# Kernel tuning notes

Hardware: AMD Instinct MI355X
Metric: run time of the kernel (lower is better)

Reference implementation:

```python
import math
import jax, jax.numpy as jnp
import numpy as np

FACTOR = 5  # must match init_kwargs factor


def setup_inputs() -> dict:
    key = jax.random.key(0)
    B, L, H, D = 4, 2048, 16, 64
    k1, k2, k3, k4 = jax.random.split(key, 4)
    q = jax.random.normal(k1, (B, L, H, D), jnp.float32)
    k = jax.random.normal(k2, (B, L, H, D), jnp.float32)
    v = jax.random.normal(k3, (B, L, H, D), jnp.float32)
    sample_k = min(FACTOR * int(np.ceil(np.log(L))), L)  # = 40
    sample_idx = jax.random.randint(k4, (L, sample_k), 0, L)
    return {"q": q, "k": k, "v": v, "sample_idx": sample_idx, "attn_mask": 0}


def reference(q, k, v, sample_idx, attn_mask):
    B, L_q, H, D = q.shape
    L_k = k.shape[1]
    qh = jnp.swapaxes(q, 1, 2)  # [B,H,L_q,D]
    kh = jnp.swapaxes(k, 1, 2)  # [B,H,L_k,D]
    vh = jnp.swapaxes(v, 1, 2)  # [B,H,L_k,D]

    u_top = min(FACTOR * int(np.ceil(np.log(L_q))), L_q)

    # --- _prob_qk: sampled QK scores and sparsity measure M ---
    # k_s[b,h,q,s,d] = kh[b,h,sample_idx[q,s],d]  (per-query random key sample)
    k_s = kh[:, :, sample_idx, :]                       # [B,H,L_q,S,D]
    qk_sample = jnp.einsum('bhqd,bhqsd->bhqs', qh, k_s)  # [B,H,L_q,S]
    M = qk_sample.max(axis=-1) - qk_sample.sum(axis=-1) / L_k  # [B,H,L_q]
    _, M_top = jax.lax.top_k(M, u_top)                   # [B,H,u]

    # gather the top-u queries
    q_red = jnp.take_along_axis(qh, M_top[..., None], axis=2)  # [B,H,u,D]

    # dense scores of selected queries against all keys
    scores = jnp.einsum('bhud,bhkd->bhuk', q_red, kh) / math.sqrt(D)
    attn = jax.nn.softmax(scores, axis=-1)                     # [B,H,u,L_k]
    ctx = jnp.einsum('bhuk,bhkd->bhud', attn, vh)              # [B,H,u,D]

    # scatter context back into v at the selected query rows (RHS uses original v,
    # matching torch fancy-index assignment semantics)
    b_idx = jnp.arange(B)[:, None, None]
    h_idx = jnp.arange(H)[None, :, None]
    out = vh.at[b_idx, h_idx, M_top].set(ctx)
    return jnp.swapaxes(out, 1, 2)  # [B,L,H,D]
```

## Files before the change

### kernel.cpp

```cpp
#include <hip/hip_runtime.h>
#include <hip/hip_bf16.h>
#include <float.h>
#include <math.h>

constexpr int B = 4;
constexpr int L = 2048;
constexpr int H = 16;
constexpr int D = 64;
constexpr int U = 40;
constexpr int UHB = 20;
constexpr int KROWS = 128;
constexpr int NRCH = 16;
constexpr int LPB = 16;
constexpr int CPB2 = 2048;

typedef float floatx4 __attribute__((ext_vector_type(4)));

template<int SKC>
__global__ __launch_bounds__(256) void compute_M_kernel2(const float* __restrict__ q,
                                                         const float* __restrict__ k,
                                                         const int* __restrict__ sidx,
                                                         float* __restrict__ M) {
    int blk = blockIdx.x;
    int xcd = blk & 7;
    int rest = blk >> 3;
    int bh_hi = rest & 7;
    int chunk = rest >> 3;
    int bh = bh_hi * 8 + xcd;
    int b = bh >> 4, h = bh & 15;

    int t = threadIdx.x;
    int lg = t >> 4;
    int dg = t & 15;

    __shared__ int s_idx[LPB * SKC];
    for (int i = t; i < LPB * SKC; i += 256)
        s_idx[i] = sidx[(size_t)(chunk * LPB) * SKC + i];
    __syncthreads();

    int l = chunk * LPB + lg;
    floatx4 qv = __builtin_nontemporal_load(
        reinterpret_cast<const floatx4*>(q + ((size_t)(b * L + l) * H + h) * D + dg * 4));

    float mx = -FLT_MAX;
    float sm = 0.f;
    #pragma unroll 4
    for (int s = 0; s < SKC; ++s) {
        int kidx = s_idx[lg * SKC + s];
        floatx4 kv = *reinterpret_cast<const floatx4*>(
            k + ((size_t)(b * L + kidx) * H + h) * D + dg * 4);
        float p = qv.x * kv.x + qv.y * kv.y + qv.z * kv.z + qv.w * kv.w;
        #pragma unroll
        for (int off = 8; off >= 1; off >>= 1) p += __shfl_xor(p, off, 16);
        mx = fmaxf(mx, p);
        sm += p;
    }
    if (dg == 0) {
        M[(size_t)bh * L + l] = mx - sm * (1.0f / (float)L);
    }
}

__global__ __launch_bounds__(256) void compute_M_kernel(const float* __restrict__ q,
                                                        const float* __restrict__ k,
                                                        const int* __restrict__ sidx,
                                                        float* __restrict__ M, int SK) {
    int bl = blockIdx.x;
    int b = bl / L;
    int l = bl % L;
    int t = threadIdx.x;
    int h = t >> 4;
    int dg = t & 15;

    const float* qrow = q + ((size_t)(b * L + l)) * H * D + h * D + dg * 4;
    float4 qv = *reinterpret_cast<const float4*>(qrow);

    float mx = -FLT_MAX;
    float sm = 0.f;
    for (int s = 0; s < SK; ++s) {
        int kidx = sidx[l * SK + s];
        const float* krow = k + ((size_t)(b * L + kidx)) * H * D + h * D + dg * 4;
        float4 kv = *reinterpret_cast<const float4*>(krow);
        float p = qv.x * kv.x + qv.y * kv.y + qv.z * kv.z + qv.w * kv.w;
        #pragma unroll
        for (int off = 8; off >= 1; off >>= 1) p += __shfl_xor(p, off, 16);
        mx = fmaxf(mx, p);
        sm += p;
    }
    if (dg == 0) {
        M[((size_t)(b * H + h)) * L + l] = mx - sm * (1.0f / (float)L);
    }
}

__global__ __launch_bounds__(256) void topk_copy_kernel(const float* __restrict__ M,
                                                        int* __restrict__ Mtop,
                                                        const float* __restrict__ v,
                                                        float* __restrict__ out, int n4) {
    int blk = blockIdx.x;
    int t = threadIdx.x;

    if (blk >= B * H) {
        int i = (blk - B * H) * 256 + t;
        int stride = CPB2 * 256;
        const floatx4* src = reinterpret_cast<const floatx4*>(v);
        floatx4* dst = reinterpret_cast<floatx4*>(out);
        for (; i < n4; i += stride) {
            floatx4 x = __builtin_nontemporal_load(src + i);
            __builtin_nontemporal_store(x, dst + i);
        }
        return;
    }
    if (t >= 64) return;

    int bh = blk;
    int lane = t;
    const float* m = M + (size_t)bh * L;

    float v_[32];
    #pragma unroll
    for (int j = 0; j < 32; ++j) v_[j] = m[j * 64 + lane];

    for (int u = 0; u < U; ++u) {
        float bv = -FLT_MAX;
        int bi = 0x7fffffff;
        #pragma unroll
        for (int j = 0; j < 32; ++j) {
            int idx = j * 64 + lane;
            bool take = (v_[j] > bv) || (v_[j] == bv && idx < bi);
            bv = take ? v_[j] : bv;
            bi = take ? idx : bi;
        }
        #pragma unroll
        for (int off = 1; off < 64; off <<= 1) {
            float ov = __shfl_xor(bv, off);
            int   oi = __shfl_xor(bi, off);
            bool take = (ov > bv) || (ov == bv && oi < bi);
            bv = take ? ov : bv;
            bi = take ? oi : bi;
        }
        if (lane == 0) Mtop[bh * U + u] = bi;
        #pragma unroll
        for (int j = 0; j < 32; ++j) {
            if (bi == j * 64 + lane) v_[j] = -FLT_MAX;
        }
    }
}

__global__ __launch_bounds__(256) void flash2_kernel(
        const float* __restrict__ q, const float* __restrict__ k,
        const float* __restrict__ v, const int* __restrict__ Mtop,
        float* __restrict__ pl, float* __restrict__ pacc) {
    int blk = blockIdx.x;
    int xcd = blk & 7;
    int bh = ((blk >> 3) & 7) * 8 + xcd;
    int rest = blk >> 6;
    int rch = rest >> 1;
    int uhalf = rest & 1;
    int b = bh >> 4, h = bh & 15;
    int t = threadIdx.x;

    __shared__ __align__(16) float qs[UHB][D];
    __shared__ __align__(16) float pe[UHB][KROWS];
    __shared__ float redl[4][10];

    for (int i = t; i < UHB * D; i += 256) {
        int u = i >> 6, dd = i & 63;
        int qi = Mtop[bh * U + uhalf * UHB + u];
        qs[u][dd] = q[((size_t)(b * L + qi) * H + h) * D + dd];
    }
    __syncthreads();

    int tq = t >> 7;
    int rl = t & 127;
    int w = t >> 6;

    int r = rch * KROWS + rl;
    const float4* krow = reinterpret_cast<const float4*>(k + ((size_t)(b * L + r) * H + h) * D);

    float s[10];
    #pragma unroll
    for (int uu = 0; uu < 10; ++uu) s[uu] = 0.f;
    #pragma unroll 4
    for (int j = 0; j < 16; ++j) {
        float4 kj = krow[j];
        #pragma unroll
        for (int uu = 0; uu < 10; ++uu) {
            float4 qj = reinterpret_cast<const float4*>(qs[tq * 10 + uu])[j];
            s[uu] = fmaf(kj.x, qj.x, fmaf(kj.y, qj.y, fmaf(kj.z, qj.z, fmaf(kj.w, qj.w, s[uu]))));
        }
    }

    #pragma unroll
    for (int uu = 0; uu < 10; ++uu) {
        float e = __expf(s[uu] * 0.125f);
        pe[tq * 10 + uu][rl] = e;
        float ls = e;
        #pragma unroll
        for (int off = 1; off < 64; off <<= 1) ls += __shfl_xor(ls, off);
        if ((t & 63) == 0) redl[w][uu] = ls;
    }
    __syncthreads();

    int d = t & 63;
    int ug = t >> 6;
    const float* vb = v + ((size_t)(b * L + rch * KROWS) * H + h) * D + d;
    float acc[5];
    #pragma unroll
    for (int uu = 0; uu < 5; ++uu) acc[uu] = 0.f;
    #pragma unroll 2
    for (int row = 0; row < KROWS; row += 4) {
        float v0 = vb[(size_t)(row    ) * (H * D)];
        float v1 = vb[(size_t)(row + 1) * (H * D)];
        float v2 = vb[(size_t)(row + 2) * (H * D)];
        float v3 = vb[(size_t)(row + 3) * (H * D)];
        #pragma unroll
        for (int uu = 0; uu < 5; ++uu) {
            float4 p4 = *reinterpret_cast<const float4*>(&pe[ug * 5 + uu][row]);
            acc[uu] = fmaf(p4.x, v0, fmaf(p4.y, v1, fmaf(p4.z, v2, fmaf(p4.w, v3, acc[uu]))));
        }
    }
    size_t pb0 = (size_t)bh * U + uhalf * UHB;
    #pragma unroll
    for (int uu = 0; uu < 5; ++uu) {
        pacc[((pb0 + ug * 5 + uu) * NRCH + rch) * 64 + d] = acc[uu];
    }
    if (t < UHB) {
        int tqo = t / 10, uu = t % 10;
        float plv = redl[tqo * 2][uu] + redl[tqo * 2 + 1][uu];
        pl[(pb0 + t) * NRCH + rch] = plv;
    }
}

__global__ __launch_bounds__(256) void flash_merge_kernel(
        const float* __restrict__ pl, const float* __restrict__ pacc,
        const int* __restrict__ Mtop, float* __restrict__ out) {
    int idx = blockIdx.x * 256 + threadIdx.x;
    int dd = idx & 63;
    int bhu = idx >> 6;
    int bh = bhu / U;
    int b = bh / H, h = bh % H;

    float Lsum = 0.f;
    #pragma unroll
    for (int c = 0; c < NRCH; ++c) Lsum += pl[bhu * NRCH + c];

    float acc = 0.f;
    #pragma unroll
    for (int c = 0; c < NRCH; ++c)
        acc += pacc[((size_t)bhu * NRCH + c) * 64 + dd];

    int qi = Mtop[bhu];
    out[((size_t)(b * L + qi) * H + h) * D + dd] = acc / Lsum;
}

__global__ __launch_bounds__(256) void attn_kernel_fallback(
        const float* __restrict__ q, const float* __restrict__ k,
        const float* __restrict__ v, const int* __restrict__ Mtop,
        float* __restrict__ out) {
    int blk = blockIdx.x;
    int bh = blk / U;
    int u = blk % U;
    int b = bh / H;
    int h = bh % H;
    int qi = Mtop[bh * U + u];

    __shared__ float sc[L];
    __shared__ float qsf[D];
    __shared__ float red[4];
    __shared__ float ctx_s[4][D];

    int t = threadIdx.x;
    if (t < D) qsf[t] = q[((size_t)(b * L + qi)) * H * D + h * D + t];
    __syncthreads();

    float lm = -FLT_MAX;
    for (int i = t; i < L; i += 256) {
        const float* krow = k + ((size_t)(b * L + i)) * H * D + h * D;
        float acc = 0.f;
        #pragma unroll
        for (int dd = 0; dd < D; ++dd) acc += qsf[dd] * krow[dd];
        acc *= 0.125f;
        sc[i] = acc;
        lm = fmaxf(lm, acc);
    }
    #pragma unroll
    for (int off = 32; off >= 1; off >>= 1) lm = fmaxf(lm, __shfl_xor(lm, off));
    if ((t & 63) == 0) red[t >> 6] = lm;
    __syncthreads();
    float gm = fmaxf(fmaxf(red[0], red[1]), fmaxf(red[2], red[3]));

    float ls = 0.f;
    for (int i = t; i < L; i += 256) {
        float e = expf(sc[i] - gm);
        sc[i] = e;
        ls += e;
    }
    #pragma unroll
    for (int off = 32; off >= 1; off >>= 1) ls += __shfl_xor(ls, off);
    __syncthreads();
    if ((t & 63) == 0) red[t >> 6] = ls;
    __syncthreads();
    float inv = 1.0f / (red[0] + red[1] + red[2] + red[3]);

    int d = t & 63;
    int g = t >> 6;
    float acc = 0.f;
    for (int i = g; i < L; i += 4) {
        acc += sc[i] * v[((size_t)(b * L + i)) * H * D + h * D + d];
    }
    ctx_s[g][d] = acc;
    __syncthreads();
    if (g == 0) {
        float c = (ctx_s[0][d] + ctx_s[1][d] + ctx_s[2][d] + ctx_s[3][d]) * inv;
        out[((size_t)(b * L + qi)) * H * D + h * D + d] = c;
    }
}

extern "C" void kernel_launch(void* const* d_in, const int* in_sizes, int n_in,
                              void* d_out, int out_size, void* d_ws, size_t ws_size,
                              hipStream_t stream) {
    const float* q = (const float*)d_in[0];
    const float* k = (const float*)d_in[1];
    const float* v = (const float*)d_in[2];
    const int* sidx = (const int*)d_in[3];
    float* out = (float*)d_out;

    int SK = in_sizes[3] / L;

    size_t offM = 0;
    size_t offMtop = offM + (size_t)B * H * L * sizeof(float);
    size_t offPl = (offMtop + (size_t)B * H * U * sizeof(int) + 255) & ~(size_t)255;
    size_t offPacc = (offPl + (size_t)B * H * U * NRCH * sizeof(float) + 255) & ~(size_t)255;
    size_t needFlash = offPacc + (size_t)B * H * U * NRCH * 64 * sizeof(float);

    float* M = (float*)((char*)d_ws + offM);
    int* Mtop = (int*)((char*)d_ws + offMtop);
    float* pl = (float*)((char*)d_ws + offPl);
    float* pacc = (float*)((char*)d_ws + offPacc);

    int n4 = (B * L * H * D) / 4;

    if (SK == 40) {
        compute_M_kernel2<40><<<B * H * (L / LPB), 256, 0, stream>>>(q, k, sidx, M);
    } else {
        compute_M_kernel<<<B * L, 256, 0, stream>>>(q, k, sidx, M, SK);
    }

    topk_copy_kernel<<<B * H + CPB2, 256, 0, stream>>>(M, Mtop, v, out, n4);

    if (ws_size >= needFlash) {
        flash2_kernel<<<B * H * NRCH * 2, 256, 0, stream>>>(q, k, v, Mtop, pl, pacc);
        flash_merge_kernel<<<B * H * U * 64 / 256, 256, 0, stream>>>(pl, pacc, Mtop, out);
    } else {
        attn_kernel_fallback<<<B * H * U, 256, 0, stream>>>(q, k, v, Mtop, out);
    }
}
```

Baseline: 205.5 us.

## Process all 40 queries per block with 4x5 register tiling in flash kernel

Merges the two query-half blocks into one block handling all 40 selected queries per key chunk, so K and V chunks are loaded once instead of twice. Each thread now computes a 4-row by 5-query register tile of scores, reusing each shared-memory Q load across four key rows. The PV stage uses float2 V loads and two output columns per thread. Grid size halves to 1024 blocks, which lowers parallelism, and shared memory per block grows.

```diff
diff --git a/kernel.cpp b/kernel.cpp
--- a/kernel.cpp
+++ b/kernel.cpp
@@ -8,7 +8,6 @@
 constexpr int H = 16;
 constexpr int D = 64;
 constexpr int U = 40;
-constexpr int UHB = 20;
 constexpr int KROWS = 128;
 constexpr int NRCH = 16;
 constexpr int LPB = 16;
@@ -145,88 +144,101 @@
     }
 }
 
-__global__ __launch_bounds__(256) void flash2_kernel(
+__global__ __launch_bounds__(256) void flash3_kernel(
         const float* __restrict__ q, const float* __restrict__ k,
         const float* __restrict__ v, const int* __restrict__ Mtop,
         float* __restrict__ pl, float* __restrict__ pacc) {
     int blk = blockIdx.x;
     int xcd = blk & 7;
     int bh = ((blk >> 3) & 7) * 8 + xcd;
-    int rest = blk >> 6;
-    int rch = rest >> 1;
-    int uhalf = rest & 1;
+    int rch = blk >> 6;
     int b = bh >> 4, h = bh & 15;
     int t = threadIdx.x;
 
-    __shared__ __align__(16) float qs[UHB][D];
-    __shared__ __align__(16) float pe[UHB][KROWS];
-    __shared__ float redl[4][10];
-
-    for (int i = t; i < UHB * D; i += 256) {
+    __shared__ __align__(16) float qs[U][D];
+    __shared__ __align__(16) float pe[U][KROWS];
+    __shared__ float redl[8][5];
+
+    for (int i = t; i < U * D; i += 256) {
         int u = i >> 6, dd = i & 63;
-        int qi = Mtop[bh * U + uhalf * UHB + u];
+        int qi = Mtop[bh * U + u];
         qs[u][dd] = q[((size_t)(b * L + qi) * H + h) * D + dd];
     }
     __syncthreads();
 
-    int tq = t >> 7;
-    int rl = t & 127;
-    int w = t >> 6;
-
-    int r = rch * KROWS + rl;
-    const float4* krow = reinterpret_cast<const float4*>(k + ((size_t)(b * L + r) * H + h) * D);
-
-    float s[10];
-    #pragma unroll
-    for (int uu = 0; uu < 10; ++uu) s[uu] = 0.f;
+    int rg = t & 31;
+    int ug = t >> 5;
+    int r0 = rch * KROWS + rg * 4;
+    const float* kb = k + ((size_t)(b * L + r0) * H + h) * D;
+
+    float s0[5], s1[5], s2[5], s3[5];
+    #pragma unroll
+    for (int uu = 0; uu < 5; ++uu) { s0[uu] = 0.f; s1[uu] = 0.f; s2[uu] = 0.f; s3[uu] = 0.f; }
+
     #pragma unroll 4
     for (int j = 0; j < 16; ++j) {
-        float4 kj = krow[j];
-        #pragma unroll
-        for (int uu = 0; uu < 10; ++uu) {
-            float4 qj = reinterpret_cast<const float4*>(qs[tq * 10 + uu])[j];
-            s[uu] = fmaf(kj.x, qj.x, fmaf(kj.y, qj.y, fmaf(kj.z, qj.z, fmaf(kj.w, qj.w, s[uu]))));
-        }
-    }
-
-    #pragma unroll
-    for (int uu = 0; uu < 10; ++uu) {
-        float e = __expf(s[uu] * 0.125f);
-        pe[tq * 10 + uu][rl] = e;
-        float ls = e;
-        #pragma unroll
-        for (int off = 1; off < 64; off <<= 1) ls += __shfl_xor(ls, off);
-        if ((t & 63) == 0) redl[w][uu] = ls;
-    }
-    __syncthreads();
-
-    int d = t & 63;
-    int ug = t >> 6;
+        float4 k0 = *reinterpret_cast<const float4*>(kb + 0 * (H * D) + j * 4);
+        float4 k1 = *reinterpret_cast<const float4*>(kb + 1 * (H * D) + j * 4);
+        float4 k2 = *reinterpret_cast<const float4*>(kb + 2 * (H * D) + j * 4);
+        float4 k3 = *reinterpret_cast<const float4*>(kb + 3 * (H * D) + j * 4);
+        #pragma unroll
+        for (int uu = 0; uu < 5; ++uu) {
+            float4 qj = *reinterpret_cast<const float4*>(&qs[ug * 5 + uu][j * 4]);
+            s0[uu] = fmaf(k0.x, qj.x, fmaf(k0.y, qj.y, fmaf(k0.z, qj.z, fmaf(k0.w, qj.w, s0[uu]))));
+            s1[uu] = fmaf(k1.x, qj.x, fmaf(k1.y, qj.y, fmaf(k1.z, qj.z, fmaf(k1.w, qj.w, s1[uu]))));
+            s2[uu] = fmaf(k2.x, qj.x, fmaf(k2.y, qj.y, fmaf(k2.z, qj.z, fmaf(k2.w, qj.w, s2[uu]))));
+            s3[uu] = fmaf(k3.x, qj.x, fmaf(k3.y, qj.y, fmaf(k3.z, qj.z, fmaf(k3.w, qj.w, s3[uu]))));
+        }
+    }
+
+    #pragma unroll
+    for (int uu = 0; uu < 5; ++uu) {
+        int u = ug * 5 + uu;
+        float e0 = __expf(s0[uu] * 0.125f);
+        float e1 = __expf(s1[uu] * 0.125f);
+        float e2 = __expf(s2[uu] * 0.125f);
+        float e3 = __expf(s3[uu] * 0.125f);
+        pe[u][rg * 4 + 0] = e0;
+        pe[u][rg * 4 + 1] = e1;
+        pe[u][rg * 4 + 2] = e2;
+        pe[u][rg * 4 + 3] = e3;
+        float sv = (e0 + e1) + (e2 + e3);
+        #pragma unroll
+        for (int off = 1; off <= 16; off <<= 1) sv += __shfl_xor(sv, off);
+        if ((t & 31) == 0) redl[ug][uu] = sv;
+    }
+    __syncthreads();
+
+    int d2 = t & 31;
+    int ug2 = t >> 5;
+    int d = d2 * 2;
     const float* vb = v + ((size_t)(b * L + rch * KROWS) * H + h) * D + d;
-    float acc[5];
-    #pragma unroll
-    for (int uu = 0; uu < 5; ++uu) acc[uu] = 0.f;
+    float ax[5], ay[5];
+    #pragma unroll
+    for (int uu = 0; uu < 5; ++uu) { ax[uu] = 0.f; ay[uu] = 0.f; }
     #pragma unroll 2
     for (int row = 0; row < KROWS; row += 4) {
-        float v0 = vb[(size_t)(row    ) * (H * D)];
-        float v1 = vb[(size_t)(row + 1) * (H * D)];
-        float v2 = vb[(size_t)(row + 2) * (H * D)];
-        float v3 = vb[(size_t)(row + 3) * (H * D)];
+        float2 v0 = *reinterpret_cast<const float2*>(vb + (size_t)(row + 0) * (H * D));
+        float2 v1 = *reinterpret_cast<const float2*>(vb + (size_t)(row + 1) * (H * D));
+        float2 v2 = *reinterpret_cast<const float2*>(vb + (size_t)(row + 2) * (H * D));
+        float2 v3 = *reinterpret_cast<const float2*>(vb + (size_t)(row + 3) * (H * D));
         #pragma unroll
         for (int uu = 0; uu < 5; ++uu) {
-            float4 p4 = *reinterpret_cast<const float4*>(&pe[ug * 5 + uu][row]);
-            acc[uu] = fmaf(p4.x, v0, fmaf(p4.y, v1, fmaf(p4.z, v2, fmaf(p4.w, v3, acc[uu]))));
-        }
-    }
-    size_t pb0 = (size_t)bh * U + uhalf * UHB;
+            float4 p4 = *reinterpret_cast<const float4*>(&pe[ug2 * 5 + uu][row]);
+            ax[uu] = fmaf(p4.x, v0.x, fmaf(p4.y, v1.x, fmaf(p4.z, v2.x, fmaf(p4.w, v3.x, ax[uu]))));
+            ay[uu] = fmaf(p4.x, v0.y, fmaf(p4.y, v1.y, fmaf(p4.z, v2.y, fmaf(p4.w, v3.y, ay[uu]))));
+        }
+    }
+
+    size_t pb0 = (size_t)bh * U;
     #pragma unroll
     for (int uu = 0; uu < 5; ++uu) {
-        pacc[((pb0 + ug * 5 + uu) * NRCH + rch) * 64 + d] = acc[uu];
-    }
-    if (t < UHB) {
-        int tqo = t / 10, uu = t % 10;
-        float plv = redl[tqo * 2][uu] + redl[tqo * 2 + 1][uu];
-        pl[(pb0 + t) * NRCH + rch] = plv;
+        int u = ug2 * 5 + uu;
+        float2 o; o.x = ax[uu]; o.y = ay[uu];
+        *reinterpret_cast<float2*>(&pacc[((pb0 + u) * NRCH + rch) * 64 + d]) = o;
+    }
+    if (t < U) {
+        pl[(pb0 + t) * NRCH + rch] = redl[t / 5][t % 5];
     }
 }
 
@@ -348,7 +360,7 @@
     topk_copy_kernel<<<B * H + CPB2, 256, 0, stream>>>(M, Mtop, v, out, n4);
 
     if (ws_size >= needFlash) {
-        flash2_kernel<<<B * H * NRCH * 2, 256, 0, stream>>>(q, k, v, Mtop, pl, pacc);
+        flash3_kernel<<<B * H * NRCH, 256, 0, stream>>>(q, k, v, Mtop, pl, pacc);
         flash_merge_kernel<<<B * H * U * 64 / 256, 256, 0, stream>>>(pl, pacc, Mtop, out);
     } else {
         attn_kernel_fallback<<<B * H * U, 256, 0, stream>>>(q, k, v, Mtop, out);
```

New measurement: 212.0 us. 3.2% more time.
